# Kernel optimization log

Hardware: AMD Instinct MI355X
Metric: run time of the kernel (lower is better)

Reference implementation:

```python
import jax, jax.numpy as jnp
import numpy as np

D = 256   # input_size
H = 512   # hidden_size
A = 4     # alpha_dim
K = 2 * A * A  # output values per input dim (binary=False -> 2 params)


def _masks():
    # MADE sequential-ordering masks, per DART.create_masks
    in_deg = np.arange(D)
    hid_deg = np.arange(H) % (D - 1)
    out_deg = np.arange(D) - 1  # arange(D) % D - 1
    m0 = (hid_deg[:, None] >= in_deg[None, :]).astype(np.float32)   # [H, D]
    mh = (hid_deg[:, None] >= hid_deg[None, :]).astype(np.float32)  # [H, H]
    ml = (out_deg[:, None] >= hid_deg[None, :]).astype(np.float32)  # [D, H]
    # repeat(1, K).view(-1, H): each output-dim row repeated K consecutive times
    ml = np.repeat(ml, K, axis=0)                                    # [D*K, H]
    return jnp.asarray(m0), jnp.asarray(mh), jnp.asarray(ml)


def setup_inputs() -> dict:
    key = jax.random.key(0)
    ks = jax.random.split(key, 10)
    B = 1024
    x = jax.random.normal(ks[0], (B, D), dtype=jnp.float32)
    def lin(k, out_dim, in_dim):
        s = 1.0 / np.sqrt(in_dim)
        kw, kb = jax.random.split(k)
        W = jax.random.uniform(kw, (out_dim, in_dim), jnp.float32, -s, s)
        b = jax.random.uniform(kb, (out_dim,), jnp.float32, -s, s)
        return W, b
    W0, b0 = lin(ks[1], H, D)
    W1, b1 = lin(ks[2], H, H)
    W2, b2 = lin(ks[3], H, H)
    Wout, bout = lin(ks[4], D * K, H)
    # unnormalized_log_p_alpha initialized to log(1/A)
    ulpa = jnp.full((1, D - 1, 1, A), -np.log(A), dtype=jnp.float32)
    return {"x": x, "W0": W0, "b0": b0, "W1": W1, "b1": b1,
            "W2": W2, "b2": b2, "Wout": Wout, "bout": bout, "ulpa": ulpa}


def reference(x, W0, b0, W1, b1, W2, b2, Wout, bout, ulpa):
    m0, mh, ml = _masks()
    B = x.shape[0]
    # masked MLP (MADE)
    h = jax.nn.relu(x @ (m0 * W0).T + b0)
    h = jax.nn.relu(h @ (mh * W1).T + b1)
    h = jax.nn.relu(h @ (mh * W2).T + b2)
    theta = (h @ (ml * Wout).T + bout).reshape(B, D, 2, A, A)
    mu = theta[:, :, 0]                      # [B, D, A, A]
    std = jnp.exp(theta[:, :, 1]) + 0.01     # [B, D, A, A]
    xe = x[:, :, None, None]
    # Normal log-prob
    log_px = -0.5 * jnp.square((xe - mu) / std) - jnp.log(std) - 0.5 * jnp.log(2.0 * jnp.pi)
    # normalized log p(alpha): [1, D-1, 1, A]
    lpa = jax.nn.log_softmax(ulpa, axis=-1)
    joint = log_px[:, :-1] + lpa             # [B, D-1, A, A]
    first = joint[:, 0, 0:1]                 # [B, 1, A]
    inner = jnp.swapaxes(joint[:, 1:], 0, 1)  # [D-2, B, A, A]
    # HMM-style forward recursion: stable log-domain chain matmul via scan
    def step(carry, m):
        # carry: [B, 1, A]; m: [B, A, A]
        new = jax.nn.logsumexp(carry[:, :, :, None] + m[:, None, :, :], axis=-2)
        return new, None
    carry, _ = jax.lax.scan(step, first, inner)
    last = log_px[:, -1, :, 0:1]             # [B, A, 1]
    log_p = jax.nn.logsumexp(carry[:, :, :, None] + last[:, None, :, :], axis=-2)  # [B,1,1]
    return log_p, theta
```

## Files before the change

kernel.cpp:

```cpp
#include <hip/hip_runtime.h>
#include <math.h>

#define Bsz 1024
#define Dd  256
#define Hh  512
#define NOUT 8192

typedef __attribute__((ext_vector_type(8))) short bf8_t;
typedef __attribute__((ext_vector_type(4))) float f4_t;

__device__ inline ushort f2b(float f) {
  union { float f; unsigned u; } c; c.f = f;
  unsigned r = c.u + 0x7fffu + ((c.u >> 16) & 1u);
  return (ushort)(r >> 16);
}

__device__ inline void async16(const ushort* g, ushort* l) {
  __builtin_amdgcn_global_load_lds((const __attribute__((address_space(1))) void*)g,
                                   (__attribute__((address_space(3))) void*)l, 16, 0, 0);
}

__device__ inline int mod255(int v) {
  if (v >= 510) return v - 510;
  if (v >= 255) return v - 255;
  return v;
}

__global__ __launch_bounds__(256) void prep(
    const float* __restrict__ x,  const float* __restrict__ W0,
    const float* __restrict__ W1, const float* __restrict__ W2,
    const float* __restrict__ Wout, const float* __restrict__ ulpa,
    ushort* __restrict__ xb, ushort* __restrict__ w0b, ushort* __restrict__ w1b,
    ushort* __restrict__ w2b, ushort* __restrict__ woutb,
    float* __restrict__ lpa)
{
  const int blk = blockIdx.x, tid = threadIdx.x;
  if (blk == 2496) {
    if (tid < Dd - 1) {
      float v0 = ulpa[tid * 4 + 0], v1 = ulpa[tid * 4 + 1];
      float v2 = ulpa[tid * 4 + 2], v3 = ulpa[tid * 4 + 3];
      float m = fmaxf(fmaxf(v0, v1), fmaxf(v2, v3));
      float s = __expf(v0 - m) + __expf(v1 - m) + __expf(v2 - m) + __expf(v3 - m);
      float l = m + __logf(s);
      lpa[tid * 4 + 0] = v0 - l;
      lpa[tid * 4 + 1] = v1 - l;
      lpa[tid * 4 + 2] = v2 - l;
      lpa[tid * 4 + 3] = v3 - l;
    }
    return;
  }
  const float* src; ushort* dst; int lb, mode;
  if (blk < 128)      { src = x;    dst = xb;    lb = blk;       mode = 0; }
  else if (blk < 192) { src = W0;   dst = w0b;   lb = blk - 128; mode = 1; }
  else if (blk < 320) { src = W1;   dst = w1b;   lb = blk - 192; mode = 2; }
  else if (blk < 448) { src = W2;   dst = w2b;   lb = blk - 320; mode = 2; }
  else                { src = Wout; dst = woutb; lb = blk - 448; mode = 3; }

  const int e = lb * 2048 + tid * 8;
  float4 v0 = *(const float4*)(src + e);
  float4 v1 = *(const float4*)(src + e + 4);
  float vv[8] = {v0.x, v0.y, v0.z, v0.w, v1.x, v1.y, v1.z, v1.w};
  ushort u[8];
  if (mode == 0) {
#pragma unroll
    for (int i = 0; i < 8; i++) u[i] = f2b(vv[i]);
  } else if (mode == 1) {
    int n = e >> 8, k0 = e & 255, nd = mod255(n);
#pragma unroll
    for (int i = 0; i < 8; i++) u[i] = (nd >= k0 + i) ? f2b(vv[i]) : (ushort)0;
  } else if (mode == 2) {
    int n = e >> 9, k0 = e & 511, nd = mod255(n);
#pragma unroll
    for (int i = 0; i < 8; i++) u[i] = (nd >= mod255(k0 + i)) ? f2b(vv[i]) : (ushort)0;
  } else {
    int n = e >> 9, k0 = e & 511, nd = (n >> 5) - 1;
#pragma unroll
    for (int i = 0; i < 8; i++) u[i] = (nd >= mod255(k0 + i)) ? f2b(vv[i]) : (ushort)0;
  }
  *(ushort4*)(dst + e)     = *(ushort4*)&u[0];
  *(ushort4*)(dst + e + 4) = *(ushort4*)&u[4];
}

template<int KD>
__global__ __launch_bounds__(256) void gemm_s(
    const ushort* __restrict__ A, const ushort* __restrict__ W,
    const float* __restrict__ bias, ushort* __restrict__ Ch)
{
  constexpr int NT = KD / 64;
  __shared__ ushort As[3][64 * 64];
  __shared__ ushort Bs[3][32 * 64];
  const int tid = threadIdx.x, lane = tid & 63, wave = tid >> 6;
  const int row0 = blockIdx.y * 64, col0 = blockIdx.x * 32;
  const int fm = lane & 15, qq = lane >> 4;
  const int srow = lane >> 3, qslot = lane & 7;

  f4_t acc[2];
  acc[0] = (f4_t){0.f, 0.f, 0.f, 0.f};
  acc[1] = (f4_t){0.f, 0.f, 0.f, 0.f};

  auto stage = [&](int buf, int kt) {
#pragma unroll
    for (int a = 0; a < 2; a++) {
      int rb = wave * 16 + a * 8;
      int r = rb + srow;
      int q = (qslot - r) & 7;
      async16(A + (size_t)(row0 + r) * KD + kt + q * 8, &As[buf][rb * 64]);
    }
    {
      int rb = wave * 8;
      int r = rb + srow;
      int q = (qslot - r) & 7;
      async16(W + (size_t)(col0 + r) * KD + kt + q * 8, &Bs[buf][rb * 64]);
    }
  };

  stage(0, 0);
  stage(1, 64);

#pragma unroll
  for (int i = 0; i < NT; i++) {
    if (i + 1 < NT) asm volatile("s_waitcnt vmcnt(3)" ::: "memory");
    else            asm volatile("s_waitcnt vmcnt(0)" ::: "memory");
    __builtin_amdgcn_s_barrier();
    asm volatile("" ::: "memory");
    if (i + 2 < NT) stage((i + 2) % 3, (i + 2) * 64);
    const int buf = i % 3;
#pragma unroll
    for (int t = 0; t < 2; t++) {
      int ra = wave * 16 + fm;
      int slota = ((t * 4 + qq) + ra) & 7;
      bf8_t af = *(const bf8_t*)&As[buf][ra * 64 + slota * 8];
#pragma unroll
      for (int j = 0; j < 2; j++) {
        int rb = j * 16 + fm;
        int slot = ((t * 4 + qq) + rb) & 7;
        bf8_t bf = *(const bf8_t*)&Bs[buf][rb * 64 + slot * 8];
        acc[j] = __builtin_amdgcn_mfma_f32_16x16x32_bf16(af, bf, acc[j], 0, 0, 0);
      }
    }
    asm volatile("s_waitcnt lgkmcnt(0)" ::: "memory");
  }

#pragma unroll
  for (int j = 0; j < 2; j++) {
    int col = col0 + j * 16 + fm;
    float bv = bias[col];
    int rbase = row0 + wave * 16 + qq * 4;
#pragma unroll
    for (int r = 0; r < 4; r++) {
      float t = fmaxf(acc[j][r] + bv, 0.0f);
      Ch[(size_t)(rbase + r) * Hh + col] = f2b(t);
    }
  }
}

__global__ __launch_bounds__(256) void gemm_big(
    const ushort* __restrict__ A, const ushort* __restrict__ W,
    const float* __restrict__ bias, float* __restrict__ Cf,
    int M, int N, int Kd)
{
  __shared__ ushort As[2][128 * 64];
  __shared__ ushort Bs[2][128 * 64];
  const int tid = threadIdx.x, lane = tid & 63, wave = tid >> 6;
  const int waveM = wave >> 1, waveN = wave & 1;
  const int row0 = blockIdx.y * 128, col0 = blockIdx.x * 128;
  const int fm = lane & 15, qq = lane >> 4;
  const int srow = lane >> 3, qslot = lane & 7;

  f4_t acc[4][4];
#pragma unroll
  for (int i = 0; i < 4; i++)
#pragma unroll
    for (int j = 0; j < 4; j++) acc[i][j] = (f4_t){0.f, 0.f, 0.f, 0.f};

  auto stage = [&](int buf, int kt) {
#pragma unroll
    for (int p = 0; p < 4; p++) {
      int rb = p * 32 + wave * 8;
      int r = rb + srow;
      int q = (qslot - r) & 7;
      async16(A + (size_t)(row0 + r) * Kd + kt + q * 8, &As[buf][rb * 64]);
    }
#pragma unroll
    for (int p = 0; p < 4; p++) {
      int rb = p * 32 + wave * 8;
      int r = rb + srow;
      int q = (qslot - r) & 7;
      async16(W + (size_t)(col0 + r) * Kd + kt + q * 8, &Bs[buf][rb * 64]);
    }
  };

  stage(0, 0);
  int cur = 0;
  for (int kt = 0; kt < Kd; kt += 64) {
    asm volatile("s_waitcnt vmcnt(0)" ::: "memory");
    __builtin_amdgcn_s_barrier();
    asm volatile("" ::: "memory");
    if (kt + 64 < Kd) stage(cur ^ 1, kt + 64);
#pragma unroll
    for (int t = 0; t < 2; t++) {
      bf8_t af[4], bf[4];
#pragma unroll
      for (int i = 0; i < 4; i++) {
        int r = waveM * 64 + i * 16 + fm;
        int slot = ((t * 4 + qq) + r) & 7;
        af[i] = *(const bf8_t*)&As[cur][r * 64 + slot * 8];
      }
#pragma unroll
      for (int j = 0; j < 4; j++) {
        int r = waveN * 64 + j * 16 + fm;
        int slot = ((t * 4 + qq) + r) & 7;
        bf[j] = *(const bf8_t*)&Bs[cur][r * 64 + slot * 8];
      }
#pragma unroll
      for (int i = 0; i < 4; i++)
#pragma unroll
        for (int j = 0; j < 4; j++)
          acc[i][j] = __builtin_amdgcn_mfma_f32_16x16x32_bf16(af[i], bf[j], acc[i][j], 0, 0, 0);
    }
    asm volatile("s_waitcnt lgkmcnt(0)" ::: "memory");
    cur ^= 1;
  }

#pragma unroll
  for (int j = 0; j < 4; j++) {
    int col = col0 + waveN * 64 + j * 16 + fm;
    float bv = bias[col];
#pragma unroll
    for (int i = 0; i < 4; i++) {
      int rbase = row0 + waveM * 64 + i * 16 + qq * 4;
#pragma unroll
      for (int r = 0; r < 4; r++)
        Cf[(size_t)(rbase + r) * N + col] = acc[i][j][r] + bv;
    }
  }
}

__global__ __launch_bounds__(512) void chain2(
    const float* __restrict__ x, const float* __restrict__ theta,
    const float* __restrict__ lpa, float* __restrict__ logp)
{
  __shared__ float ths[256 * 33];
  __shared__ float xs[256];
  __shared__ float lps[255 * 5];
  __shared__ float TA[32][16];
  __shared__ float TB[16][16];

  const int b = blockIdx.x;
  const int tid = threadIdx.x;
  const float C0 = 0.91893853320467274178f;

  const float4* src = (const float4*)(theta + (size_t)b * NOUT);
#pragma unroll
  for (int it = 0; it < 4; it++) {
    int t = tid + it * 512;
    float4 v = src[t];
    int d = t >> 3, c = (t & 7) * 4;
    float* p = &ths[d * 33 + c];
    p[0] = v.x; p[1] = v.y; p[2] = v.z; p[3] = v.w;
  }
  if (tid < 64) ((float4*)xs)[tid] = ((const float4*)(x + (size_t)b * Dd))[tid];
  if (tid < 255) {
    float4 v = ((const float4*)lpa)[tid];
    float* p = &lps[tid * 5];
    p[0] = v.x; p[1] = v.y; p[2] = v.z; p[3] = v.w;
  }
  __syncthreads();

  const int seg = tid >> 4, e = tid & 15, ii = e >> 2, jj = e & 3;
  const int base = (tid & 63) & ~15;
  const int d0 = 1 + seg * 8;
  const int d1 = min(d0 + 8, Dd - 1);

  auto stepm = [&](int d) -> float {
    float mu = ths[d * 33 + e];
    float ls = ths[d * 33 + 16 + e];
    float s  = __expf(ls) + 0.01f;
    float z  = (xs[d] - mu) * __builtin_amdgcn_rcpf(s);
    return -0.5f * z * z - __logf(s) - C0 + lps[d * 5 + jj];
  };

  float T = stepm(d0);
  for (int d = d0 + 1; d < d1; d++) {
    float m_ = stepm(d);
    float v0 = __shfl(T, base + ii * 4 + 0) + __shfl(m_, base + 0 * 4 + jj);
    float v1 = __shfl(T, base + ii * 4 + 1) + __shfl(m_, base + 1 * 4 + jj);
    float v2 = __shfl(T, base + ii * 4 + 2) + __shfl(m_, base + 2 * 4 + jj);
    float v3 = __shfl(T, base + ii * 4 + 3) + __shfl(m_, base + 3 * 4 + jj);
    float mx = fmaxf(fmaxf(v0, v1), fmaxf(v2, v3));
    float s  = __expf(v0 - mx) + __expf(v1 - mx) + __expf(v2 - mx) + __expf(v3 - mx);
    T = mx + __logf(s);
  }
  TA[seg][e] = T;
  __syncthreads();

  float (*cur)[16] = TA;
  float (*nxt)[16] = TB;
#pragma unroll
  for (int n = 16; n >= 1; n >>= 1) {
    if (tid < n * 16) {
      int p = tid >> 4, ee = tid & 15, i2 = ee >> 2, j2 = ee & 3;
      const float* L = cur[2 * p];
      const float* R = cur[2 * p + 1];
      float v0 = L[i2 * 4 + 0] + R[0 * 4 + j2];
      float v1 = L[i2 * 4 + 1] + R[1 * 4 + j2];
      float v2 = L[i2 * 4 + 2] + R[2 * 4 + j2];
      float v3 = L[i2 * 4 + 3] + R[3 * 4 + j2];
      float mx = fmaxf(fmaxf(v0, v1), fmaxf(v2, v3));
      float ss = __expf(v0 - mx) + __expf(v1 - mx) + __expf(v2 - mx) + __expf(v3 - mx);
      nxt[p][ee] = mx + __logf(ss);
    }
    __syncthreads();
    float (*tmp)[16] = cur; cur = nxt; nxt = tmp;
  }

  if (tid < 16) {
    int i = tid >> 2, j = tid & 3;
    float mu0 = ths[i], ls0 = ths[16 + i];
    float s0 = __expf(ls0) + 0.01f;
    float z0 = (xs[0] - mu0) * __builtin_amdgcn_rcpf(s0);
    float c0 = -0.5f * z0 * z0 - __logf(s0) - C0 + lps[i];
    float muL = ths[255 * 33 + j * 4];
    float lsL = ths[255 * 33 + 16 + j * 4];
    float sL = __expf(lsL) + 0.01f;
    float zL = (xs[255] - muL) * __builtin_amdgcn_rcpf(sL);
    float lL = -0.5f * zL * zL - __logf(sL) - C0;
    float v = c0 + cur[0][tid] + lL;
    float mx = fmaxf(v, __shfl_xor(v, 1));
    mx = fmaxf(mx, __shfl_xor(mx, 2));
    mx = fmaxf(mx, __shfl_xor(mx, 4));
    mx = fmaxf(mx, __shfl_xor(mx, 8));
    float ee = __expf(v - mx);
    ee += __shfl_xor(ee, 1);
    ee += __shfl_xor(ee, 2);
    ee += __shfl_xor(ee, 4);
    ee += __shfl_xor(ee, 8);
    if (tid == 0) logp[b] = mx + __logf(ee);
  }
}

extern "C" void kernel_launch(void* const* d_in, const int* in_sizes, int n_in,
                              void* d_out, int out_size, void* d_ws, size_t ws_size,
                              hipStream_t stream)
{
  const float* x    = (const float*)d_in[0];
  const float* W0   = (const float*)d_in[1];
  const float* b0   = (const float*)d_in[2];
  const float* W1   = (const float*)d_in[3];
  const float* b1   = (const float*)d_in[4];
  const float* W2   = (const float*)d_in[5];
  const float* b2   = (const float*)d_in[6];
  const float* Wout = (const float*)d_in[7];
  const float* bout = (const float*)d_in[8];
  const float* ulpa = (const float*)d_in[9];

  float* out   = (float*)d_out;
  float* logp  = out;
  float* theta = out + Bsz;

  ushort* ws    = (ushort*)d_ws;
  ushort* xb    = ws;
  ushort* w0b   = xb + 262144;
  ushort* w1b   = w0b + 131072;
  ushort* w2b   = w1b + 262144;
  ushort* woutb = w2b + 262144;
  ushort* h0    = woutb + 4194304;
  ushort* h1    = h0 + 524288;
  ushort* h2    = h1 + 524288;
  float*  lpa   = (float*)(h2 + 524288);

  prep<<<2497, 256, 0, stream>>>(x, W0, W1, W2, Wout, ulpa,
                                 xb, w0b, w1b, w2b, woutb, lpa);
  gemm_s<Dd><<<dim3(16, 16), 256, 0, stream>>>(xb, w0b, b0, h0);
  gemm_s<Hh><<<dim3(16, 16), 256, 0, stream>>>(h0, w1b, b1, h1);
  gemm_s<Hh><<<dim3(16, 16), 256, 0, stream>>>(h1, w2b, b2, h2);
  gemm_big<<<dim3(NOUT / 128, Bsz / 128), 256, 0, stream>>>(h2, woutb, bout, theta, Bsz, NOUT, Hh);
  chain2<<<Bsz, 512, 0, stream>>>(x, theta, lpa, logp);
}
```

Before: 136.1 us.

## Fuse all stages into one persistent kernel with software grid barriers

Replaces the six separate launches (prep, three small GEMMs, the big output GEMM, the chain) with a single persistent 256-block kernel that separates the phases with atomic-counter grid barriers, plus a memset to reset the counters. The aim is to remove per-launch overhead and the idle gaps between dependent kernels. The chain stage is reworked so each block handles 4 batch rows with 256 threads and 16-step segments, and the big GEMM loops over 2 tiles per block. In exchange it forces one block per CU, which lowers occupancy for the large GEMM and the chain. The barriers also depend on all 256 blocks being co-resident and have a timeout guard that can silently break correctness.

Result: slower. 294.7 us (+116.6%).

```diff
diff --git a/kernel.cpp b/kernel.cpp
--- a/kernel.cpp
+++ b/kernel.cpp
@@ -26,71 +26,89 @@
   return v;
 }
 
-__global__ __launch_bounds__(256) void prep(
+__device__ inline void gridbar(unsigned* bar, unsigned target) {
+  __syncthreads();
+  if (threadIdx.x == 0) {
+    __threadfence();
+    atomicAdd(bar, 1u);
+    int guard = 0;
+    while (__hip_atomic_load(bar, __ATOMIC_RELAXED, __HIP_MEMORY_SCOPE_AGENT) < target) {
+      __builtin_amdgcn_s_sleep(2);
+      if (++guard > (1 << 22)) break;
+    }
+  }
+  __syncthreads();
+  __threadfence();
+}
+
+__device__ __forceinline__ void prep_body(
     const float* __restrict__ x,  const float* __restrict__ W0,
     const float* __restrict__ W1, const float* __restrict__ W2,
     const float* __restrict__ Wout, const float* __restrict__ ulpa,
     ushort* __restrict__ xb, ushort* __restrict__ w0b, ushort* __restrict__ w1b,
     ushort* __restrict__ w2b, ushort* __restrict__ woutb,
-    float* __restrict__ lpa)
-{
-  const int blk = blockIdx.x, tid = threadIdx.x;
-  if (blk == 2496) {
-    if (tid < Dd - 1) {
-      float v0 = ulpa[tid * 4 + 0], v1 = ulpa[tid * 4 + 1];
-      float v2 = ulpa[tid * 4 + 2], v3 = ulpa[tid * 4 + 3];
-      float m = fmaxf(fmaxf(v0, v1), fmaxf(v2, v3));
-      float s = __expf(v0 - m) + __expf(v1 - m) + __expf(v2 - m) + __expf(v3 - m);
-      float l = m + __logf(s);
-      lpa[tid * 4 + 0] = v0 - l;
-      lpa[tid * 4 + 1] = v1 - l;
-      lpa[tid * 4 + 2] = v2 - l;
-      lpa[tid * 4 + 3] = v3 - l;
-    }
-    return;
-  }
-  const float* src; ushort* dst; int lb, mode;
-  if (blk < 128)      { src = x;    dst = xb;    lb = blk;       mode = 0; }
-  else if (blk < 192) { src = W0;   dst = w0b;   lb = blk - 128; mode = 1; }
-  else if (blk < 320) { src = W1;   dst = w1b;   lb = blk - 192; mode = 2; }
-  else if (blk < 448) { src = W2;   dst = w2b;   lb = blk - 320; mode = 2; }
-  else                { src = Wout; dst = woutb; lb = blk - 448; mode = 3; }
-
-  const int e = lb * 2048 + tid * 8;
-  float4 v0 = *(const float4*)(src + e);
-  float4 v1 = *(const float4*)(src + e + 4);
-  float vv[8] = {v0.x, v0.y, v0.z, v0.w, v1.x, v1.y, v1.z, v1.w};
-  ushort u[8];
-  if (mode == 0) {
-#pragma unroll
-    for (int i = 0; i < 8; i++) u[i] = f2b(vv[i]);
-  } else if (mode == 1) {
-    int n = e >> 8, k0 = e & 255, nd = mod255(n);
-#pragma unroll
-    for (int i = 0; i < 8; i++) u[i] = (nd >= k0 + i) ? f2b(vv[i]) : (ushort)0;
-  } else if (mode == 2) {
-    int n = e >> 9, k0 = e & 511, nd = mod255(n);
-#pragma unroll
-    for (int i = 0; i < 8; i++) u[i] = (nd >= mod255(k0 + i)) ? f2b(vv[i]) : (ushort)0;
-  } else {
-    int n = e >> 9, k0 = e & 511, nd = (n >> 5) - 1;
-#pragma unroll
-    for (int i = 0; i < 8; i++) u[i] = (nd >= mod255(k0 + i)) ? f2b(vv[i]) : (ushort)0;
-  }
-  *(ushort4*)(dst + e)     = *(ushort4*)&u[0];
-  *(ushort4*)(dst + e + 4) = *(ushort4*)&u[4];
+    float* __restrict__ lpa, int blk)
+{
+  const int tid = threadIdx.x;
+  for (int w = blk; w < 2497; w += 256) {
+    if (w == 2496) {
+      if (tid < Dd - 1) {
+        float v0 = ulpa[tid * 4 + 0], v1 = ulpa[tid * 4 + 1];
+        float v2 = ulpa[tid * 4 + 2], v3 = ulpa[tid * 4 + 3];
+        float m = fmaxf(fmaxf(v0, v1), fmaxf(v2, v3));
+        float s = __expf(v0 - m) + __expf(v1 - m) + __expf(v2 - m) + __expf(v3 - m);
+        float l = m + __logf(s);
+        lpa[tid * 4 + 0] = v0 - l;
+        lpa[tid * 4 + 1] = v1 - l;
+        lpa[tid * 4 + 2] = v2 - l;
+        lpa[tid * 4 + 3] = v3 - l;
+      }
+      continue;
+    }
+    const float* src; ushort* dst; int lb, mode;
+    if (w < 128)      { src = x;    dst = xb;    lb = w;       mode = 0; }
+    else if (w < 192) { src = W0;   dst = w0b;   lb = w - 128; mode = 1; }
+    else if (w < 320) { src = W1;   dst = w1b;   lb = w - 192; mode = 2; }
+    else if (w < 448) { src = W2;   dst = w2b;   lb = w - 320; mode = 2; }
+    else              { src = Wout; dst = woutb; lb = w - 448; mode = 3; }
+
+    const int e = lb * 2048 + tid * 8;
+    float4 v0 = *(const float4*)(src + e);
+    float4 v1 = *(const float4*)(src + e + 4);
+    float vv[8] = {v0.x, v0.y, v0.z, v0.w, v1.x, v1.y, v1.z, v1.w};
+    ushort u[8];
+    if (mode == 0) {
+#pragma unroll
+      for (int i = 0; i < 8; i++) u[i] = f2b(vv[i]);
+    } else if (mode == 1) {
+      int n = e >> 8, k0 = e & 255, nd = mod255(n);
+#pragma unroll
+      for (int i = 0; i < 8; i++) u[i] = (nd >= k0 + i) ? f2b(vv[i]) : (ushort)0;
+    } else if (mode == 2) {
+      int n = e >> 9, k0 = e & 511, nd = mod255(n);
+#pragma unroll
+      for (int i = 0; i < 8; i++) u[i] = (nd >= mod255(k0 + i)) ? f2b(vv[i]) : (ushort)0;
+    } else {
+      int n = e >> 9, k0 = e & 511, nd = (n >> 5) - 1;
+#pragma unroll
+      for (int i = 0; i < 8; i++) u[i] = (nd >= mod255(k0 + i)) ? f2b(vv[i]) : (ushort)0;
+    }
+    *(ushort4*)(dst + e)     = *(ushort4*)&u[0];
+    *(ushort4*)(dst + e + 4) = *(ushort4*)&u[4];
+  }
 }
 
 template<int KD>
-__global__ __launch_bounds__(256) void gemm_s(
+__device__ __forceinline__ void gemm_s_body(
     const ushort* __restrict__ A, const ushort* __restrict__ W,
-    const float* __restrict__ bias, ushort* __restrict__ Ch)
+    const float* __restrict__ bias, ushort* __restrict__ Ch,
+    int blk, ushort* smem)
 {
   constexpr int NT = KD / 64;
-  __shared__ ushort As[3][64 * 64];
-  __shared__ ushort Bs[3][32 * 64];
+  ushort* As = smem;
+  ushort* Bs = smem + 3 * 4096;
   const int tid = threadIdx.x, lane = tid & 63, wave = tid >> 6;
-  const int row0 = blockIdx.y * 64, col0 = blockIdx.x * 32;
+  const int row0 = (blk >> 4) * 64, col0 = (blk & 15) * 32;
   const int fm = lane & 15, qq = lane >> 4;
   const int srow = lane >> 3, qslot = lane & 7;
 
@@ -104,13 +122,13 @@
       int rb = wave * 16 + a * 8;
       int r = rb + srow;
       int q = (qslot - r) & 7;
-      async16(A + (size_t)(row0 + r) * KD + kt + q * 8, &As[buf][rb * 64]);
+      async16(A + (size_t)(row0 + r) * KD + kt + q * 8, As + buf * 4096 + rb * 64);
     }
     {
       int rb = wave * 8;
       int r = rb + srow;
       int q = (qslot - r) & 7;
-      async16(W + (size_t)(col0 + r) * KD + kt + q * 8, &Bs[buf][rb * 64]);
+      async16(W + (size_t)(col0 + r) * KD + kt + q * 8, Bs + buf * 2048 + rb * 64);
     }
   };
 
@@ -129,12 +147,12 @@
     for (int t = 0; t < 2; t++) {
       int ra = wave * 16 + fm;
       int slota = ((t * 4 + qq) + ra) & 7;
-      bf8_t af = *(const bf8_t*)&As[buf][ra * 64 + slota * 8];
+      bf8_t af = *(const bf8_t*)(As + buf * 4096 + ra * 64 + slota * 8);
 #pragma unroll
       for (int j = 0; j < 2; j++) {
         int rb = j * 16 + fm;
         int slot = ((t * 4 + qq) + rb) & 7;
-        bf8_t bf = *(const bf8_t*)&Bs[buf][rb * 64 + slot * 8];
+        bf8_t bf = *(const bf8_t*)(Bs + buf * 2048 + rb * 64 + slot * 8);
         acc[j] = __builtin_amdgcn_mfma_f32_16x16x32_bf16(af, bf, acc[j], 0, 0, 0);
       }
     }
@@ -154,16 +172,17 @@
   }
 }
 
-__global__ __launch_bounds__(256) void gemm_big(
+__device__ __forceinline__ void gemm_big_body(
     const ushort* __restrict__ A, const ushort* __restrict__ W,
     const float* __restrict__ bias, float* __restrict__ Cf,
-    int M, int N, int Kd)
-{
-  __shared__ ushort As[2][128 * 64];
-  __shared__ ushort Bs[2][128 * 64];
+    int tileid, ushort* smem)
+{
+  const int Kd = Hh, N = NOUT;
+  ushort* As = smem;
+  ushort* Bs = smem + 2 * 8192;
   const int tid = threadIdx.x, lane = tid & 63, wave = tid >> 6;
   const int waveM = wave >> 1, waveN = wave & 1;
-  const int row0 = blockIdx.y * 128, col0 = blockIdx.x * 128;
+  const int row0 = (tileid >> 6) * 128, col0 = (tileid & 63) * 128;
   const int fm = lane & 15, qq = lane >> 4;
   const int srow = lane >> 3, qslot = lane & 7;
 
@@ -179,14 +198,14 @@
       int rb = p * 32 + wave * 8;
       int r = rb + srow;
       int q = (qslot - r) & 7;
-      async16(A + (size_t)(row0 + r) * Kd + kt + q * 8, &As[buf][rb * 64]);
+      async16(A + (size_t)(row0 + r) * Kd + kt + q * 8, As + buf * 8192 + rb * 64);
     }
 #pragma unroll
     for (int p = 0; p < 4; p++) {
       int rb = p * 32 + wave * 8;
       int r = rb + srow;
       int q = (qslot - r) & 7;
-      async16(W + (size_t)(col0 + r) * Kd + kt + q * 8, &Bs[buf][rb * 64]);
+      async16(W + (size_t)(col0 + r) * Kd + kt + q * 8, Bs + buf * 8192 + rb * 64);
     }
   };
 
@@ -204,13 +223,13 @@
       for (int i = 0; i < 4; i++) {
         int r = waveM * 64 + i * 16 + fm;
         int slot = ((t * 4 + qq) + r) & 7;
-        af[i] = *(const bf8_t*)&As[cur][r * 64 + slot * 8];
+        af[i] = *(const bf8_t*)(As + cur * 8192 + r * 64 + slot * 8);
       }
 #pragma unroll
       for (int j = 0; j < 4; j++) {
         int r = waveN * 64 + j * 16 + fm;
         int slot = ((t * 4 + qq) + r) & 7;
-        bf[j] = *(const bf8_t*)&Bs[cur][r * 64 + slot * 8];
+        bf[j] = *(const bf8_t*)(Bs + cur * 8192 + r * 64 + slot * 8);
       }
 #pragma unroll
       for (int i = 0; i < 4; i++)
@@ -236,107 +255,147 @@
   }
 }
 
-__global__ __launch_bounds__(512) void chain2(
+__device__ __forceinline__ void chain_body(
     const float* __restrict__ x, const float* __restrict__ theta,
-    const float* __restrict__ lpa, float* __restrict__ logp)
-{
-  __shared__ float ths[256 * 33];
-  __shared__ float xs[256];
-  __shared__ float lps[255 * 5];
-  __shared__ float TA[32][16];
-  __shared__ float TB[16][16];
-
-  const int b = blockIdx.x;
+    const float* __restrict__ lpa, float* __restrict__ logp,
+    int blk, ushort* smem_u)
+{
+  float* fs  = (float*)smem_u;
+  float* ths = fs;
+  float* xs  = fs + 8448;
+  float* lps = fs + 8704;
+  float (*TA)[16] = (float(*)[16])(fs + 9984);
+  float (*TB)[16] = (float(*)[16])(fs + 10240);
   const int tid = threadIdx.x;
   const float C0 = 0.91893853320467274178f;
 
-  const float4* src = (const float4*)(theta + (size_t)b * NOUT);
-#pragma unroll
-  for (int it = 0; it < 4; it++) {
-    int t = tid + it * 512;
-    float4 v = src[t];
-    int d = t >> 3, c = (t & 7) * 4;
-    float* p = &ths[d * 33 + c];
-    p[0] = v.x; p[1] = v.y; p[2] = v.z; p[3] = v.w;
-  }
-  if (tid < 64) ((float4*)xs)[tid] = ((const float4*)(x + (size_t)b * Dd))[tid];
   if (tid < 255) {
     float4 v = ((const float4*)lpa)[tid];
     float* p = &lps[tid * 5];
     p[0] = v.x; p[1] = v.y; p[2] = v.z; p[3] = v.w;
   }
+
+  for (int s = 0; s < 4; s++) {
+    const int b = blk * 4 + s;
+    __syncthreads();
+    const float4* src = (const float4*)(theta + (size_t)b * NOUT);
+#pragma unroll
+    for (int it = 0; it < 8; it++) {
+      int t = tid + it * 256;
+      float4 v = src[t];
+      int d = t >> 3, c = (t & 7) * 4;
+      float* p = &ths[d * 33 + c];
+      p[0] = v.x; p[1] = v.y; p[2] = v.z; p[3] = v.w;
+    }
+    if (tid < 64) ((float4*)xs)[tid] = ((const float4*)(x + (size_t)b * Dd))[tid];
+    __syncthreads();
+
+    const int seg = tid >> 4, e = tid & 15, ii = e >> 2, jj = e & 3;
+    const int base = (tid & 63) & ~15;
+    const int d0 = 1 + seg * 16;
+    const int d1 = min(d0 + 16, Dd - 1);
+
+    auto stepm = [&](int d) -> float {
+      float mu = ths[d * 33 + e];
+      float ls = ths[d * 33 + 16 + e];
+      float sv = __expf(ls) + 0.01f;
+      float z  = (xs[d] - mu) * __builtin_amdgcn_rcpf(sv);
+      return -0.5f * z * z - __logf(sv) - C0 + lps[d * 5 + jj];
+    };
+
+    float T = stepm(d0);
+    for (int d = d0 + 1; d < d1; d++) {
+      float m_ = stepm(d);
+      float v0 = __shfl(T, base + ii * 4 + 0) + __shfl(m_, base + 0 * 4 + jj);
+      float v1 = __shfl(T, base + ii * 4 + 1) + __shfl(m_, base + 1 * 4 + jj);
+      float v2 = __shfl(T, base + ii * 4 + 2) + __shfl(m_, base + 2 * 4 + jj);
+      float v3 = __shfl(T, base + ii * 4 + 3) + __shfl(m_, base + 3 * 4 + jj);
+      float mx = fmaxf(fmaxf(v0, v1), fmaxf(v2, v3));
+      float sm = __expf(v0 - mx) + __expf(v1 - mx) + __expf(v2 - mx) + __expf(v3 - mx);
+      T = mx + __logf(sm);
+    }
+    TA[seg][e] = T;
+    __syncthreads();
+
+    float (*cur)[16] = TA;
+    float (*nxt)[16] = TB;
+#pragma unroll
+    for (int n = 8; n >= 1; n >>= 1) {
+      if (tid < n * 16) {
+        int p = tid >> 4, ee = tid & 15, i2 = ee >> 2, j2 = ee & 3;
+        const float* L = cur[2 * p];
+        const float* R = cur[2 * p + 1];
+        float v0 = L[i2 * 4 + 0] + R[0 * 4 + j2];
+        float v1 = L[i2 * 4 + 1] + R[1 * 4 + j2];
+        float v2 = L[i2 * 4 + 2] + R[2 * 4 + j2];
+        float v3 = L[i2 * 4 + 3] + R[3 * 4 + j2];
+        float mx = fmaxf(fmaxf(v0, v1), fmaxf(v2, v3));
+        float ss = __expf(v0 - mx) + __expf(v1 - mx) + __expf(v2 - mx) + __expf(v3 - mx);
+        nxt[p][ee] = mx + __logf(ss);
+      }
+      __syncthreads();
+      float (*tmp)[16] = cur; cur = nxt; nxt = tmp;
+    }
+
+    if (tid < 16) {
+      int i = tid >> 2, j = tid & 3;
+      float mu0 = ths[i], ls0 = ths[16 + i];
+      float s0 = __expf(ls0) + 0.01f;
+      float z0 = (xs[0] - mu0) * __builtin_amdgcn_rcpf(s0);
+      float c0 = -0.5f * z0 * z0 - __logf(s0) - C0 + lps[i];
+      float muL = ths[255 * 33 + j * 4];
+      float lsL = ths[255 * 33 + 16 + j * 4];
+      float sL = __expf(lsL) + 0.01f;
+      float zL = (xs[255] - muL) * __builtin_amdgcn_rcpf(sL);
+      float lL = -0.5f * zL * zL - __logf(sL) - C0;
+      float v = c0 + cur[0][tid] + lL;
+      float mx = fmaxf(v, __shfl_xor(v, 1));
+      mx = fmaxf(mx, __shfl_xor(mx, 2));
+      mx = fmaxf(mx, __shfl_xor(mx, 4));
+      mx = fmaxf(mx, __shfl_xor(mx, 8));
+      float ee = __expf(v - mx);
+      ee += __shfl_xor(ee, 1);
+      ee += __shfl_xor(ee, 2);
+      ee += __shfl_xor(ee, 4);
+      ee += __shfl_xor(ee, 8);
+      if (tid == 0) logp[b] = mx + __logf(ee);
+    }
+  }
+}
+
+__global__ __launch_bounds__(256, 1) void fused(
+    const float* __restrict__ x,  const float* __restrict__ W0,
+    const float* __restrict__ W1, const float* __restrict__ W2,
+    const float* __restrict__ Wout, const float* __restrict__ ulpa,
+    const float* __restrict__ b0, const float* __restrict__ b1,
+    const float* __restrict__ b2, const float* __restrict__ bout,
+    ushort* __restrict__ xb, ushort* __restrict__ w0b, ushort* __restrict__ w1b,
+    ushort* __restrict__ w2b, ushort* __restrict__ woutb,
+    ushort* __restrict__ h0, ushort* __restrict__ h1, ushort* __restrict__ h2,
+    float* __restrict__ lpa, float* __restrict__ theta, float* __restrict__ logp,
+    unsigned* __restrict__ bar)
+{
+  __shared__ __align__(16) ushort smem[32768];
+  const int blk = blockIdx.x;
+
+  prep_body(x, W0, W1, W2, Wout, ulpa, xb, w0b, w1b, w2b, woutb, lpa, blk);
+  gridbar(bar + 0, 256);
+
+  gemm_s_body<Dd>(xb, w0b, b0, h0, blk, smem);
+  gridbar(bar + 1, 256);
+
+  gemm_s_body<Hh>(h0, w1b, b1, h1, blk, smem);
+  gridbar(bar + 2, 256);
+
+  gemm_s_body<Hh>(h1, w2b, b2, h2, blk, smem);
+  gridbar(bar + 3, 256);
+
+  gemm_big_body(h2, woutb, bout, theta, blk, smem);
   __syncthreads();
-
-  const int seg = tid >> 4, e = tid & 15, ii = e >> 2, jj = e & 3;
-  const int base = (tid & 63) & ~15;
-  const int d0 = 1 + seg * 8;
-  const int d1 = min(d0 + 8, Dd - 1);
-
-  auto stepm = [&](int d) -> float {
-    float mu = ths[d * 33 + e];
-    float ls = ths[d * 33 + 16 + e];
-    float s  = __expf(ls) + 0.01f;
-    float z  = (xs[d] - mu) * __builtin_amdgcn_rcpf(s);
-    return -0.5f * z * z - __logf(s) - C0 + lps[d * 5 + jj];
-  };
-
-  float T = stepm(d0);
-  for (int d = d0 + 1; d < d1; d++) {
-    float m_ = stepm(d);
-    float v0 = __shfl(T, base + ii * 4 + 0) + __shfl(m_, base + 0 * 4 + jj);
-    float v1 = __shfl(T, base + ii * 4 + 1) + __shfl(m_, base + 1 * 4 + jj);
-    float v2 = __shfl(T, base + ii * 4 + 2) + __shfl(m_, base + 2 * 4 + jj);
-    float v3 = __shfl(T, base + ii * 4 + 3) + __shfl(m_, base + 3 * 4 + jj);
-    float mx = fmaxf(fmaxf(v0, v1), fmaxf(v2, v3));
-    float s  = __expf(v0 - mx) + __expf(v1 - mx) + __expf(v2 - mx) + __expf(v3 - mx);
-    T = mx + __logf(s);
-  }
-  TA[seg][e] = T;
-  __syncthreads();
-
-  float (*cur)[16] = TA;
-  float (*nxt)[16] = TB;
-#pragma unroll
-  for (int n = 16; n >= 1; n >>= 1) {
-    if (tid < n * 16) {
-      int p = tid >> 4, ee = tid & 15, i2 = ee >> 2, j2 = ee & 3;
-      const float* L = cur[2 * p];
-      const float* R = cur[2 * p + 1];
-      float v0 = L[i2 * 4 + 0] + R[0 * 4 + j2];
-      float v1 = L[i2 * 4 + 1] + R[1 * 4 + j2];
-      float v2 = L[i2 * 4 + 2] + R[2 * 4 + j2];
-      float v3 = L[i2 * 4 + 3] + R[3 * 4 + j2];
-      float mx = fmaxf(fmaxf(v0, v1), fmaxf(v2, v3));
-      float ss = __expf(v0 - mx) + __expf(v1 - mx) + __expf(v2 - mx) + __expf(v3 - mx);
-      nxt[p][ee] = mx + __logf(ss);
-    }
-    __syncthreads();
-    float (*tmp)[16] = cur; cur = nxt; nxt = tmp;
-  }
-
-  if (tid < 16) {
-    int i = tid >> 2, j = tid & 3;
-    float mu0 = ths[i], ls0 = ths[16 + i];
-    float s0 = __expf(ls0) + 0.01f;
-    float z0 = (xs[0] - mu0) * __builtin_amdgcn_rcpf(s0);
-    float c0 = -0.5f * z0 * z0 - __logf(s0) - C0 + lps[i];
-    float muL = ths[255 * 33 + j * 4];
-    float lsL = ths[255 * 33 + 16 + j * 4];
-    float sL = __expf(lsL) + 0.01f;
-    float zL = (xs[255] - muL) * __builtin_amdgcn_rcpf(sL);
-    float lL = -0.5f * zL * zL - __logf(sL) - C0;
-    float v = c0 + cur[0][tid] + lL;
-    float mx = fmaxf(v, __shfl_xor(v, 1));
-    mx = fmaxf(mx, __shfl_xor(mx, 2));
-    mx = fmaxf(mx, __shfl_xor(mx, 4));
-    mx = fmaxf(mx, __shfl_xor(mx, 8));
-    float ee = __expf(v - mx);
-    ee += __shfl_xor(ee, 1);
-    ee += __shfl_xor(ee, 2);
-    ee += __shfl_xor(ee, 4);
-    ee += __shfl_xor(ee, 8);
-    if (tid == 0) logp[b] = mx + __logf(ee);
-  }
+  gemm_big_body(h2, woutb, bout, theta, blk + 256, smem);
+  gridbar(bar + 4, 256);
+
+  chain_body(x, theta, lpa, logp, blk, smem);
 }
 
 extern "C" void kernel_launch(void* const* d_in, const int* in_sizes, int n_in,
@@ -368,12 +427,11 @@
   ushort* h1    = h0 + 524288;
   ushort* h2    = h1 + 524288;
   float*  lpa   = (float*)(h2 + 524288);
-
-  prep<<<2497, 256, 0, stream>>>(x, W0, W1, W2, Wout, ulpa,
-                                 xb, w0b, w1b, w2b, woutb, lpa);
-  gemm_s<Dd><<<dim3(16, 16), 256, 0, stream>>>(xb, w0b, b0, h0);
-  gemm_s<Hh><<<dim3(16, 16), 256, 0, stream>>>(h0, w1b, b1, h1);
-  gemm_s<Hh><<<dim3(16, 16), 256, 0, stream>>>(h1, w2b, b2, h2);
-  gemm_big<<<dim3(NOUT / 128, Bsz / 128), 256, 0, stream>>>(h2, woutb, bout, theta, Bsz, NOUT, Hh);
-  chain2<<<Bsz, 512, 0, stream>>>(x, theta, lpa, logp);
-}
+  unsigned* bar = (unsigned*)(lpa + 1024);
+
+  hipMemsetAsync((void*)bar, 0, 64, stream);
+  fused<<<256, 256, 0, stream>>>(x, W0, W1, W2, Wout, ulpa,
+                                 b0, b1, b2, bout,
+                                 xb, w0b, w1b, w2b, woutb,
+                                 h0, h1, h2, lpa, theta, logp, bar);
+}
```

## Fuse Gaussian log-prob into output GEMM epilogue and shrink hidden GEMM tiles

Applied to the files above, without the earlier changes.

The output GEMM epilogue now computes the per-element Normal log-probability plus log p(alpha) directly from its accumulators. It writes a compact joint buffer (half the size of theta), so the chain kernel reads 16 floats per dimension instead of 32 and skips the exp/log/rcp work. Separately, the hidden-layer GEMM tiles shrink from 64x32 to 32x32, with each wave owning one 16x16 sub-tile. This doubles the grid for more parallelism across CUs. The cost is an extra global write of the joint buffer, strided x reads in the big GEMM epilogue, and higher register pressure there.

Result: no change. 138.5 us (+1.8%).

```diff
diff --git a/kernel.cpp b/kernel.cpp
--- a/kernel.cpp
+++ b/kernel.cpp
@@ -87,21 +87,19 @@
     const float* __restrict__ bias, ushort* __restrict__ Ch)
 {
   constexpr int NT = KD / 64;
-  __shared__ ushort As[3][64 * 64];
+  __shared__ ushort As[3][32 * 64];
   __shared__ ushort Bs[3][32 * 64];
   const int tid = threadIdx.x, lane = tid & 63, wave = tid >> 6;
-  const int row0 = blockIdx.y * 64, col0 = blockIdx.x * 32;
+  const int row0 = blockIdx.y * 32, col0 = blockIdx.x * 32;
+  const int rt = wave >> 1, ct = wave & 1;
   const int fm = lane & 15, qq = lane >> 4;
   const int srow = lane >> 3, qslot = lane & 7;
 
-  f4_t acc[2];
-  acc[0] = (f4_t){0.f, 0.f, 0.f, 0.f};
-  acc[1] = (f4_t){0.f, 0.f, 0.f, 0.f};
+  f4_t acc = (f4_t){0.f, 0.f, 0.f, 0.f};
 
   auto stage = [&](int buf, int kt) {
-#pragma unroll
-    for (int a = 0; a < 2; a++) {
-      int rb = wave * 16 + a * 8;
+    {
+      int rb = wave * 8;
       int r = rb + srow;
       int q = (qslot - r) & 7;
       async16(A + (size_t)(row0 + r) * KD + kt + q * 8, &As[buf][rb * 64]);
@@ -119,7 +117,7 @@
 
 #pragma unroll
   for (int i = 0; i < NT; i++) {
-    if (i + 1 < NT) asm volatile("s_waitcnt vmcnt(3)" ::: "memory");
+    if (i + 1 < NT) asm volatile("s_waitcnt vmcnt(2)" ::: "memory");
     else            asm volatile("s_waitcnt vmcnt(0)" ::: "memory");
     __builtin_amdgcn_s_barrier();
     asm volatile("" ::: "memory");
@@ -127,28 +125,24 @@
     const int buf = i % 3;
 #pragma unroll
     for (int t = 0; t < 2; t++) {
-      int ra = wave * 16 + fm;
+      int ra = rt * 16 + fm;
       int slota = ((t * 4 + qq) + ra) & 7;
       bf8_t af = *(const bf8_t*)&As[buf][ra * 64 + slota * 8];
-#pragma unroll
-      for (int j = 0; j < 2; j++) {
-        int rb = j * 16 + fm;
-        int slot = ((t * 4 + qq) + rb) & 7;
-        bf8_t bf = *(const bf8_t*)&Bs[buf][rb * 64 + slot * 8];
-        acc[j] = __builtin_amdgcn_mfma_f32_16x16x32_bf16(af, bf, acc[j], 0, 0, 0);
-      }
+      int rb = ct * 16 + fm;
+      int slotb = ((t * 4 + qq) + rb) & 7;
+      bf8_t bf = *(const bf8_t*)&Bs[buf][rb * 64 + slotb * 8];
+      acc = __builtin_amdgcn_mfma_f32_16x16x32_bf16(af, bf, acc, 0, 0, 0);
     }
     asm volatile("s_waitcnt lgkmcnt(0)" ::: "memory");
   }
 
-#pragma unroll
-  for (int j = 0; j < 2; j++) {
-    int col = col0 + j * 16 + fm;
+  {
+    int col = col0 + ct * 16 + fm;
     float bv = bias[col];
-    int rbase = row0 + wave * 16 + qq * 4;
+    int rbase = row0 + rt * 16 + qq * 4;
 #pragma unroll
     for (int r = 0; r < 4; r++) {
-      float t = fmaxf(acc[j][r] + bv, 0.0f);
+      float t = fmaxf(acc[r] + bv, 0.0f);
       Ch[(size_t)(rbase + r) * Hh + col] = f2b(t);
     }
   }
@@ -157,6 +151,8 @@
 __global__ __launch_bounds__(256) void gemm_big(
     const ushort* __restrict__ A, const ushort* __restrict__ W,
     const float* __restrict__ bias, float* __restrict__ Cf,
+    const float* __restrict__ x, const float* __restrict__ lpa,
+    float* __restrict__ jointbuf,
     int M, int N, int Kd)
 {
   __shared__ ushort As[2][128 * 64];
@@ -166,6 +162,7 @@
   const int row0 = blockIdx.y * 128, col0 = blockIdx.x * 128;
   const int fm = lane & 15, qq = lane >> 4;
   const int srow = lane >> 3, qslot = lane & 7;
+  const float C0 = 0.91893853320467274178f;
 
   f4_t acc[4][4];
 #pragma unroll
@@ -234,35 +231,50 @@
         Cf[(size_t)(rbase + r) * N + col] = acc[i][j][r] + bv;
     }
   }
+
+  const int d_base = (col0 + waveN * 64) >> 5;
+  const int jj = fm & 3;
+#pragma unroll
+  for (int dd = 0; dd < 2; dd++) {
+    const int d = d_base + dd;
+    const int cm = col0 + waveN * 64 + dd * 32 + fm;
+    const float bmu = bias[cm];
+    const float bls = bias[cm + 16];
+    const float lpav = (d < Dd - 1) ? lpa[d * 4 + jj] : 0.0f;
+#pragma unroll
+    for (int i = 0; i < 4; i++) {
+      const int rbase = row0 + waveM * 64 + i * 16 + qq * 4;
+#pragma unroll
+      for (int r = 0; r < 4; r++) {
+        const int row = rbase + r;
+        float mu = acc[i][2 * dd][r] + bmu;
+        float ls = acc[i][2 * dd + 1][r] + bls;
+        float sv = __expf(ls) + 0.01f;
+        float z  = (x[(size_t)row * Dd + d] - mu) * __builtin_amdgcn_rcpf(sv);
+        jointbuf[(size_t)row * 4096 + d * 16 + fm] =
+            -0.5f * z * z - __logf(sv) - C0 + lpav;
+      }
+    }
+  }
 }
 
 __global__ __launch_bounds__(512) void chain2(
-    const float* __restrict__ x, const float* __restrict__ theta,
-    const float* __restrict__ lpa, float* __restrict__ logp)
-{
-  __shared__ float ths[256 * 33];
-  __shared__ float xs[256];
-  __shared__ float lps[255 * 5];
+    const float* __restrict__ jointbuf, float* __restrict__ logp)
+{
+  __shared__ float js[256 * 17];
   __shared__ float TA[32][16];
   __shared__ float TB[16][16];
 
   const int b = blockIdx.x;
   const int tid = threadIdx.x;
-  const float C0 = 0.91893853320467274178f;
-
-  const float4* src = (const float4*)(theta + (size_t)b * NOUT);
-#pragma unroll
-  for (int it = 0; it < 4; it++) {
+
+  const float4* src = (const float4*)(jointbuf + (size_t)b * 4096);
+#pragma unroll
+  for (int it = 0; it < 2; it++) {
     int t = tid + it * 512;
     float4 v = src[t];
-    int d = t >> 3, c = (t & 7) * 4;
-    float* p = &ths[d * 33 + c];
-    p[0] = v.x; p[1] = v.y; p[2] = v.z; p[3] = v.w;
-  }
-  if (tid < 64) ((float4*)xs)[tid] = ((const float4*)(x + (size_t)b * Dd))[tid];
-  if (tid < 255) {
-    float4 v = ((const float4*)lpa)[tid];
-    float* p = &lps[tid * 5];
+    int d = t >> 2, c = (t & 3) * 4;
+    float* p = &js[d * 17 + c];
     p[0] = v.x; p[1] = v.y; p[2] = v.z; p[3] = v.w;
   }
   __syncthreads();
@@ -272,17 +284,9 @@
   const int d0 = 1 + seg * 8;
   const int d1 = min(d0 + 8, Dd - 1);
 
-  auto stepm = [&](int d) -> float {
-    float mu = ths[d * 33 + e];
-    float ls = ths[d * 33 + 16 + e];
-    float s  = __expf(ls) + 0.01f;
-    float z  = (xs[d] - mu) * __builtin_amdgcn_rcpf(s);
-    return -0.5f * z * z - __logf(s) - C0 + lps[d * 5 + jj];
-  };
-
-  float T = stepm(d0);
+  float T = js[d0 * 17 + e];
   for (int d = d0 + 1; d < d1; d++) {
-    float m_ = stepm(d);
+    float m_ = js[d * 17 + e];
     float v0 = __shfl(T, base + ii * 4 + 0) + __shfl(m_, base + 0 * 4 + jj);
     float v1 = __shfl(T, base + ii * 4 + 1) + __shfl(m_, base + 1 * 4 + jj);
     float v2 = __shfl(T, base + ii * 4 + 2) + __shfl(m_, base + 2 * 4 + jj);
@@ -316,15 +320,8 @@
 
   if (tid < 16) {
     int i = tid >> 2, j = tid & 3;
-    float mu0 = ths[i], ls0 = ths[16 + i];
-    float s0 = __expf(ls0) + 0.01f;
-    float z0 = (xs[0] - mu0) * __builtin_amdgcn_rcpf(s0);
-    float c0 = -0.5f * z0 * z0 - __logf(s0) - C0 + lps[i];
-    float muL = ths[255 * 33 + j * 4];
-    float lsL = ths[255 * 33 + 16 + j * 4];
-    float sL = __expf(lsL) + 0.01f;
-    float zL = (xs[255] - muL) * __builtin_amdgcn_rcpf(sL);
-    float lL = -0.5f * zL * zL - __logf(sL) - C0;
+    float c0 = js[i];
+    float lL = js[255 * 17 + j * 4];
     float v = c0 + cur[0][tid] + lL;
     float mx = fmaxf(v, __shfl_xor(v, 1));
     mx = fmaxf(mx, __shfl_xor(mx, 2));
@@ -368,12 +365,14 @@
   ushort* h1    = h0 + 524288;
   ushort* h2    = h1 + 524288;
   float*  lpa   = (float*)(h2 + 524288);
+  float*  jointbuf = lpa + 1024;
 
   prep<<<2497, 256, 0, stream>>>(x, W0, W1, W2, Wout, ulpa,
                                  xb, w0b, w1b, w2b, woutb, lpa);
-  gemm_s<Dd><<<dim3(16, 16), 256, 0, stream>>>(xb, w0b, b0, h0);
-  gemm_s<Hh><<<dim3(16, 16), 256, 0, stream>>>(h0, w1b, b1, h1);
-  gemm_s<Hh><<<dim3(16, 16), 256, 0, stream>>>(h1, w2b, b2, h2);
-  gemm_big<<<dim3(NOUT / 128, Bsz / 128), 256, 0, stream>>>(h2, woutb, bout, theta, Bsz, NOUT, Hh);
-  chain2<<<Bsz, 512, 0, stream>>>(x, theta, lpa, logp);
-}
+  gemm_s<Dd><<<dim3(16, 32), 256, 0, stream>>>(xb, w0b, b0, h0);
+  gemm_s<Hh><<<dim3(16, 32), 256, 0, stream>>>(h0, w1b, b1, h1);
+  gemm_s<Hh><<<dim3(16, 32), 256, 0, stream>>>(h1, w2b, b2, h2);
+  gemm_big<<<dim3(NOUT / 128, Bsz / 128), 256, 0, stream>>>(
+      h2, woutb, bout, theta, x, lpa, jointbuf, Bsz, NOUT, Hh);
+  chain2<<<Bsz, 512, 0, stream>>>(jointbuf, logp);
+}
```

## Fold weight conversion into the small GEMM kernels and drop the prep launch

Applied to the files above, without the earlier changes.

Removes the separate prep kernel. The first layer GEMM now converts x and the masked W0 to bf16 directly while filling shared memory. Conversion of W1, W2, Wout and the log-softmax of ulpa are spread across the tail of the three small GEMM kernels, so each weight is ready before the kernel that uses it. This saves one launch and the xb/w0b round trip through global memory. The cost is extra tail work in each small GEMM, with Wout conversion split into chunks by offset.

Result: slower. 142.0 us (+4.4%).

```diff
diff --git a/kernel.cpp b/kernel.cpp
--- a/kernel.cpp
+++ b/kernel.cpp
@@ -26,65 +26,129 @@
   return v;
 }
 
-__global__ __launch_bounds__(256) void prep(
-    const float* __restrict__ x,  const float* __restrict__ W0,
-    const float* __restrict__ W1, const float* __restrict__ W2,
-    const float* __restrict__ Wout, const float* __restrict__ ulpa,
-    ushort* __restrict__ xb, ushort* __restrict__ w0b, ushort* __restrict__ w1b,
-    ushort* __restrict__ w2b, ushort* __restrict__ woutb,
-    float* __restrict__ lpa)
-{
-  const int blk = blockIdx.x, tid = threadIdx.x;
-  if (blk == 2496) {
-    if (tid < Dd - 1) {
-      float v0 = ulpa[tid * 4 + 0], v1 = ulpa[tid * 4 + 1];
-      float v2 = ulpa[tid * 4 + 2], v3 = ulpa[tid * 4 + 3];
-      float m = fmaxf(fmaxf(v0, v1), fmaxf(v2, v3));
-      float s = __expf(v0 - m) + __expf(v1 - m) + __expf(v2 - m) + __expf(v3 - m);
-      float l = m + __logf(s);
-      lpa[tid * 4 + 0] = v0 - l;
-      lpa[tid * 4 + 1] = v1 - l;
-      lpa[tid * 4 + 2] = v2 - l;
-      lpa[tid * 4 + 3] = v3 - l;
-    }
-    return;
-  }
-  const float* src; ushort* dst; int lb, mode;
-  if (blk < 128)      { src = x;    dst = xb;    lb = blk;       mode = 0; }
-  else if (blk < 192) { src = W0;   dst = w0b;   lb = blk - 128; mode = 1; }
-  else if (blk < 320) { src = W1;   dst = w1b;   lb = blk - 192; mode = 2; }
-  else if (blk < 448) { src = W2;   dst = w2b;   lb = blk - 320; mode = 2; }
-  else                { src = Wout; dst = woutb; lb = blk - 448; mode = 3; }
-
-  const int e = lb * 2048 + tid * 8;
+__device__ inline void conv_chunk_m2(const float* __restrict__ src,
+                                     ushort* __restrict__ dst, int cid) {
+  const int e = cid * 2048 + threadIdx.x * 8;
   float4 v0 = *(const float4*)(src + e);
   float4 v1 = *(const float4*)(src + e + 4);
   float vv[8] = {v0.x, v0.y, v0.z, v0.w, v1.x, v1.y, v1.z, v1.w};
+  int n = e >> 9, k0 = e & 511, nd = mod255(n);
   ushort u[8];
-  if (mode == 0) {
-#pragma unroll
-    for (int i = 0; i < 8; i++) u[i] = f2b(vv[i]);
-  } else if (mode == 1) {
-    int n = e >> 8, k0 = e & 255, nd = mod255(n);
-#pragma unroll
-    for (int i = 0; i < 8; i++) u[i] = (nd >= k0 + i) ? f2b(vv[i]) : (ushort)0;
-  } else if (mode == 2) {
-    int n = e >> 9, k0 = e & 511, nd = mod255(n);
-#pragma unroll
-    for (int i = 0; i < 8; i++) u[i] = (nd >= mod255(k0 + i)) ? f2b(vv[i]) : (ushort)0;
-  } else {
-    int n = e >> 9, k0 = e & 511, nd = (n >> 5) - 1;
-#pragma unroll
-    for (int i = 0; i < 8; i++) u[i] = (nd >= mod255(k0 + i)) ? f2b(vv[i]) : (ushort)0;
-  }
+#pragma unroll
+  for (int i = 0; i < 8; i++) u[i] = (nd >= mod255(k0 + i)) ? f2b(vv[i]) : (ushort)0;
   *(ushort4*)(dst + e)     = *(ushort4*)&u[0];
   *(ushort4*)(dst + e + 4) = *(ushort4*)&u[4];
+}
+
+__device__ inline void conv_chunk_m3(const float* __restrict__ src,
+                                     ushort* __restrict__ dst, int cid) {
+  const int e = cid * 2048 + threadIdx.x * 8;
+  float4 v0 = *(const float4*)(src + e);
+  float4 v1 = *(const float4*)(src + e + 4);
+  float vv[8] = {v0.x, v0.y, v0.z, v0.w, v1.x, v1.y, v1.z, v1.w};
+  int n = e >> 9, k0 = e & 511, nd = (n >> 5) - 1;
+  ushort u[8];
+#pragma unroll
+  for (int i = 0; i < 8; i++) u[i] = (nd >= mod255(k0 + i)) ? f2b(vv[i]) : (ushort)0;
+  *(ushort4*)(dst + e)     = *(ushort4*)&u[0];
+  *(ushort4*)(dst + e + 4) = *(ushort4*)&u[4];
+}
+
+__global__ __launch_bounds__(256) void gemm0(
+    const float* __restrict__ x, const float* __restrict__ W0,
+    const float* __restrict__ b0, ushort* __restrict__ h0,
+    const float* __restrict__ W1, ushort* __restrict__ w1b,
+    const float* __restrict__ Wout, ushort* __restrict__ woutb,
+    const float* __restrict__ ulpa, float* __restrict__ lpa)
+{
+  __shared__ ushort As[4 * 64 * 64];
+  __shared__ ushort Bs[4 * 32 * 64];
+  const int tid = threadIdx.x, lane = tid & 63, wave = tid >> 6;
+  const int row0 = blockIdx.y * 64, col0 = blockIdx.x * 32;
+  const int fm = lane & 15, qq = lane >> 4;
+
+#pragma unroll
+  for (int it = 0; it < 16; it++) {
+    int f = it * 256 + tid;
+    int r = f >> 6, k4 = (f & 63) << 2;
+    float4 v = *(const float4*)(x + (size_t)(row0 + r) * Dd + k4);
+    ushort4 u;
+    u.x = f2b(v.x); u.y = f2b(v.y); u.z = f2b(v.z); u.w = f2b(v.w);
+    int t = k4 >> 6, q = (k4 >> 3) & 7, half = (k4 >> 2) & 1;
+    *(ushort4*)&As[(t * 64 + r) * 64 + ((q + r) & 7) * 8 + half * 4] = u;
+  }
+#pragma unroll
+  for (int it = 0; it < 8; it++) {
+    int f = it * 256 + tid;
+    int r = f >> 6, k4 = (f & 63) << 2;
+    int n = col0 + r, nd = mod255(n);
+    float4 v = *(const float4*)(W0 + (size_t)n * Dd + k4);
+    ushort4 u;
+    u.x = (nd >= k4 + 0) ? f2b(v.x) : (ushort)0;
+    u.y = (nd >= k4 + 1) ? f2b(v.y) : (ushort)0;
+    u.z = (nd >= k4 + 2) ? f2b(v.z) : (ushort)0;
+    u.w = (nd >= k4 + 3) ? f2b(v.w) : (ushort)0;
+    int t = k4 >> 6, q = (k4 >> 3) & 7, half = (k4 >> 2) & 1;
+    *(ushort4*)&Bs[(t * 32 + r) * 64 + ((q + r) & 7) * 8 + half * 4] = u;
+  }
+  __syncthreads();
+
+  f4_t acc[2];
+  acc[0] = (f4_t){0.f, 0.f, 0.f, 0.f};
+  acc[1] = (f4_t){0.f, 0.f, 0.f, 0.f};
+#pragma unroll
+  for (int t4 = 0; t4 < 4; t4++) {
+#pragma unroll
+    for (int t = 0; t < 2; t++) {
+      int ra = wave * 16 + fm;
+      int slota = ((t * 4 + qq) + ra) & 7;
+      bf8_t af = *(const bf8_t*)&As[(t4 * 64 + ra) * 64 + slota * 8];
+#pragma unroll
+      for (int j = 0; j < 2; j++) {
+        int rb = j * 16 + fm;
+        int slot = ((t * 4 + qq) + rb) & 7;
+        bf8_t bf = *(const bf8_t*)&Bs[(t4 * 32 + rb) * 64 + slot * 8];
+        acc[j] = __builtin_amdgcn_mfma_f32_16x16x32_bf16(af, bf, acc[j], 0, 0, 0);
+      }
+    }
+  }
+
+#pragma unroll
+  for (int j = 0; j < 2; j++) {
+    int col = col0 + j * 16 + fm;
+    float bv = b0[col];
+    int rbase = row0 + wave * 16 + qq * 4;
+#pragma unroll
+    for (int r = 0; r < 4; r++) {
+      float t = fmaxf(acc[j][r] + bv, 0.0f);
+      h0[(size_t)(rbase + r) * Hh + col] = f2b(t);
+    }
+  }
+
+  const int blk = blockIdx.y * 16 + blockIdx.x;
+  if (blk < 128) conv_chunk_m2(W1, w1b, blk);
+  for (int cid = blk; cid < 683; cid += 256)
+    conv_chunk_m3(Wout, woutb, cid);
+  if (blk == 255 && tid < Dd - 1) {
+    float v0 = ulpa[tid * 4 + 0], v1 = ulpa[tid * 4 + 1];
+    float v2 = ulpa[tid * 4 + 2], v3 = ulpa[tid * 4 + 3];
+    float m = fmaxf(fmaxf(v0, v1), fmaxf(v2, v3));
+    float s = __expf(v0 - m) + __expf(v1 - m) + __expf(v2 - m) + __expf(v3 - m);
+    float l = m + __logf(s);
+    lpa[tid * 4 + 0] = v0 - l;
+    lpa[tid * 4 + 1] = v1 - l;
+    lpa[tid * 4 + 2] = v2 - l;
+    lpa[tid * 4 + 3] = v3 - l;
+  }
 }
 
 template<int KD>
 __global__ __launch_bounds__(256) void gemm_s(
     const ushort* __restrict__ A, const ushort* __restrict__ W,
-    const float* __restrict__ bias, ushort* __restrict__ Ch)
+    const float* __restrict__ bias, ushort* __restrict__ Ch,
+    const float* __restrict__ cw_src, ushort* __restrict__ cw_dst, int cw_nch,
+    const float* __restrict__ wo_src, ushort* __restrict__ wo_dst,
+    int wo_off, int wo_nch)
 {
   constexpr int NT = KD / 64;
   __shared__ ushort As[3][64 * 64];
@@ -152,6 +216,11 @@
       Ch[(size_t)(rbase + r) * Hh + col] = f2b(t);
     }
   }
+
+  const int blk = blockIdx.y * gridDim.x + blockIdx.x;
+  if (cw_src != nullptr && blk < cw_nch) conv_chunk_m2(cw_src, cw_dst, blk);
+  for (int cid = blk; cid < wo_nch; cid += 256)
+    conv_chunk_m3(wo_src, wo_dst, wo_off + cid);
 }
 
 __global__ __launch_bounds__(256) void gemm_big(
@@ -359,9 +428,7 @@
   float* theta = out + Bsz;
 
   ushort* ws    = (ushort*)d_ws;
-  ushort* xb    = ws;
-  ushort* w0b   = xb + 262144;
-  ushort* w1b   = w0b + 131072;
+  ushort* w1b   = ws;
   ushort* w2b   = w1b + 262144;
   ushort* woutb = w2b + 262144;
   ushort* h0    = woutb + 4194304;
@@ -369,11 +436,15 @@
   ushort* h2    = h1 + 524288;
   float*  lpa   = (float*)(h2 + 524288);
 
-  prep<<<2497, 256, 0, stream>>>(x, W0, W1, W2, Wout, ulpa,
-                                 xb, w0b, w1b, w2b, woutb, lpa);
-  gemm_s<Dd><<<dim3(16, 16), 256, 0, stream>>>(xb, w0b, b0, h0);
-  gemm_s<Hh><<<dim3(16, 16), 256, 0, stream>>>(h0, w1b, b1, h1);
-  gemm_s<Hh><<<dim3(16, 16), 256, 0, stream>>>(h1, w2b, b2, h2);
-  gemm_big<<<dim3(NOUT / 128, Bsz / 128), 256, 0, stream>>>(h2, woutb, bout, theta, Bsz, NOUT, Hh);
+  gemm0<<<dim3(16, 16), 256, 0, stream>>>(x, W0, b0, h0,
+                                          W1, w1b, Wout, woutb, ulpa, lpa);
+  gemm_s<Hh><<<dim3(16, 16), 256, 0, stream>>>(h0, w1b, b1, h1,
+                                               W2, w2b, 128,
+                                               Wout, woutb, 683, 683);
+  gemm_s<Hh><<<dim3(16, 16), 256, 0, stream>>>(h1, w2b, b2, h2,
+                                               nullptr, nullptr, 0,
+                                               Wout, woutb, 1366, 682);
+  gemm_big<<<dim3(NOUT / 128, Bsz / 128), 256, 0, stream>>>(
+      h2, woutb, bout, theta, Bsz, NOUT, Hh);
   chain2<<<Bsz, 512, 0, stream>>>(x, theta, lpa, logp);
 }
```
